# Optimization experiments

Hardware: AMD Instinct MI355X
Metric: run time of the kernel (lower is better)

The kernel has to match this reference:

```python
import jax, jax.numpy as jnp
import numpy as np

B, T, D = 2, 2048, 512
H, W = 8, 32
d = D // H


def setup_inputs() -> dict:
    key = jax.random.key(0)
    ks = jax.random.split(key, 9)
    s = 1.0 / np.sqrt(D)
    return {
        "x": jax.random.normal(ks[0], (B, T, D), dtype=jnp.float32),
        "wq": jax.random.normal(ks[1], (D, D), dtype=jnp.float32) * s,
        "bq": jnp.zeros((D,), dtype=jnp.float32),
        "wk": jax.random.normal(ks[2], (D, D), dtype=jnp.float32) * s,
        "bk": jnp.zeros((D,), dtype=jnp.float32),
        "wv": jax.random.normal(ks[3], (D, D), dtype=jnp.float32) * s,
        "bv": jnp.zeros((D,), dtype=jnp.float32),
        "wo": jax.random.normal(ks[4], (D, D), dtype=jnp.float32) * s,
        "bo": jnp.zeros((D,), dtype=jnp.float32),
    }


def _local_attn(x, wq, bq, wk, bk, wv, bv, wo, bo):
    Bx, Tx, Dx = x.shape
    # projections (weights stored as [D_in, D_out])
    Q = (x @ wq + bq).reshape(Bx, Tx, H, d).transpose(0, 2, 1, 3)  # [B,H,T,d]
    K = (x @ wk + bk).reshape(Bx, Tx, H, d).transpose(0, 2, 1, 3)
    V = (x @ wv + bv).reshape(Bx, Tx, H, d).transpose(0, 2, 1, 3)
    # zero-pad time axis by W on both sides (matches F.pad value=0; NO masking,
    # padded zero keys get score 0 and participate in softmax like the original)
    Kp = jnp.pad(K, ((0, 0), (0, 0), (W, W), (0, 0)))  # [B,H,T+2W,d]
    Vp = jnp.pad(V, ((0, 0), (0, 0), (W, W), (0, 0)))
    idx = jnp.arange(Tx)[:, None] + jnp.arange(2 * W + 1)[None, :]  # [T, 2W+1]
    K_loc = Kp[:, :, idx, :]  # [B,H,T,2W+1,d]
    V_loc = Vp[:, :, idx, :]
    scores = jnp.einsum("bhtd,bhtwd->bhtw", Q, K_loc) / jnp.sqrt(jnp.asarray(d, x.dtype))
    attn = jax.nn.softmax(scores, axis=-1)
    out = jnp.einsum("bhtw,bhtwd->bhtd", attn, V_loc)  # [B,H,T,d]
    out = out.transpose(0, 2, 1, 3).reshape(Bx, Tx, Dx)
    return out @ wo + bo


def reference(x, wq, bq, wk, bk, wv, bv, wo, bo):
    return _local_attn(x, wq, bq, wk, bk, wv, bv, wo, bo)
```

## Files before the change

### kernel.cpp

```cpp
#include <hip/hip_runtime.h>

using f16x8 = __attribute__((ext_vector_type(8))) _Float16;
using f16x4 = __attribute__((ext_vector_type(4))) _Float16;
using f32x4 = __attribute__((ext_vector_type(4))) float;

#define T_SEQ 2048
#define D_MODEL 512
#define NH 8
#define HD 64
#define NB 2
#define M_ROWS (NB * T_SEQ)

#define GLOAD_LDS16(g, l)                                              \
  __builtin_amdgcn_global_load_lds(                                    \
      (const __attribute__((address_space(1))) void*)(g),              \
      (__attribute__((address_space(3))) void*)(l), 16, 0, 0)

__global__ __launch_bounds__(256) void cvt_all(
    const float* __restrict__ x, const float* __restrict__ wq,
    const float* __restrict__ wk, const float* __restrict__ wv,
    const float* __restrict__ wo, const float* __restrict__ bq,
    const float* __restrict__ bk, const float* __restrict__ bv,
    _Float16* __restrict__ xh, _Float16* __restrict__ wT,
    float* __restrict__ bias3) {
  int bid = blockIdx.x;
  int i = threadIdx.x;
  if (bid < 2048) {
    int idx = (bid * 256 + i) * 4;
    float4 v = *(const float4*)(x + idx);
    f16x4 h;
    h[0] = (_Float16)v.x; h[1] = (_Float16)v.y;
    h[2] = (_Float16)v.z; h[3] = (_Float16)v.w;
    *(f16x4*)(xh + idx) = h;
    return;
  }
  bid -= 2048;
  const int z = bid >> 8;
  const int by = (bid >> 4) & 15;
  const int bx = bid & 15;
  const float* w = z == 0 ? wq : z == 1 ? wk : z == 2 ? wv : wo;
  __shared__ float t[32][33];
  int r0 = by * 32, c0 = bx * 32;
#pragma unroll
  for (int p = 0; p < 4; ++p) {
    int e = p * 256 + i;
    int row = e >> 5, col = e & 31;
    t[row][col] = w[(size_t)(r0 + row) * D_MODEL + c0 + col];
  }
  __syncthreads();
  _Float16* o = wT + (size_t)z * D_MODEL * D_MODEL;
#pragma unroll
  for (int p = 0; p < 4; ++p) {
    int e = p * 256 + i;
    int orow = e >> 5, ocol = e & 31;
    o[(size_t)(c0 + orow) * D_MODEL + r0 + ocol] = (_Float16)t[ocol][orow];
  }
  if (bx == 0 && by == 0 && z < 3) {
    const float* bb = z == 0 ? bq : z == 1 ? bk : bv;
#pragma unroll
    for (int p = 0; p < 2; ++p)
      bias3[z * D_MODEL + p * 256 + i] = bb[p * 256 + i];
  }
}

template <int OUT_F32>
__global__ __launch_bounds__(256) void gemm_bt(
    const _Float16* __restrict__ A, const _Float16* __restrict__ BtBase,
    const float* __restrict__ biasBase, void* outBase) {
  const int z = blockIdx.z;
  const _Float16* Bt = BtBase + (size_t)z * D_MODEL * D_MODEL;
  const float* bias = biasBase + z * D_MODEL;
  const int m0 = blockIdx.y * 128;
  const int n0 = blockIdx.x * 128;
  __shared__ _Float16 At[128 * 32];
  __shared__ _Float16 Bts[128 * 32];
  const int tid = threadIdx.x;
  const int l = tid & 63;
  const int wv = tid >> 6;
  const int wm = wv >> 1, wn = wv & 1;
  const int r16 = l & 15, g4 = l >> 4;
  f32x4 acc[4][4] = {};
  for (int k0 = 0; k0 < D_MODEL; k0 += 32) {
#pragma unroll
    for (int cc = 0; cc < 2; ++cc) {
      int c = tid + cc * 256;
      int row = c >> 2, part = c & 3;
      int wbase = (wv * 64 + cc * 256) * 8;
      GLOAD_LDS16(&A[(size_t)(m0 + row) * D_MODEL + k0 + part * 8],
                  &At[wbase]);
      GLOAD_LDS16(&Bt[(size_t)(n0 + row) * D_MODEL + k0 + part * 8],
                  &Bts[wbase]);
    }
    __syncthreads();
    f16x8 a[4], b[4];
#pragma unroll
    for (int mf = 0; mf < 4; ++mf)
      a[mf] = *(const f16x8*)&At[(wm * 64 + mf * 16 + r16) * 32 + g4 * 8];
#pragma unroll
    for (int nf = 0; nf < 4; ++nf)
      b[nf] = *(const f16x8*)&Bts[(wn * 64 + nf * 16 + r16) * 32 + g4 * 8];
#pragma unroll
    for (int mf = 0; mf < 4; ++mf)
#pragma unroll
      for (int nf = 0; nf < 4; ++nf)
        acc[mf][nf] = __builtin_amdgcn_mfma_f32_16x16x32_f16(
            a[mf], b[nf], acc[mf][nf], 0, 0, 0);
    __syncthreads();
  }
#pragma unroll
  for (int mf = 0; mf < 4; ++mf) {
#pragma unroll
    for (int nf = 0; nf < 4; ++nf) {
      int col = n0 + wn * 64 + nf * 16 + r16;
      float bs = bias[col];
#pragma unroll
      for (int r = 0; r < 4; ++r) {
        int rowi = m0 + wm * 64 + mf * 16 + g4 * 4 + r;
        float v = acc[mf][nf][r] + bs;
        if (OUT_F32)
          ((float*)outBase)[(size_t)rowi * D_MODEL + col] = v;
        else
          ((_Float16*)outBase)[(size_t)z * M_ROWS * D_MODEL +
                               (size_t)rowi * D_MODEL + col] = (_Float16)v;
      }
    }
  }
}

__global__ __launch_bounds__(256) void local_attn(
    const _Float16* __restrict__ Q, const _Float16* __restrict__ K,
    const _Float16* __restrict__ V, _Float16* __restrict__ att) {
  const int t0 = blockIdx.x * 64;
  const int h = blockIdx.y;
  const int b = blockIdx.z;
  const int k0 = t0 - 32;
  __shared__ _Float16 Qs[64 * 64];
  __shared__ _Float16 Ks[128 * 64];
  __shared__ _Float16 Vt[64 * 128];
  __shared__ _Float16 Ps[64 * 128];
  const int tid = threadIdx.x;
  const int l = tid & 63;
  const int wv = tid >> 6;
  const size_t colbase = (size_t)h * HD;
#pragma unroll
  for (int cc = 0; cc < 2; ++cc) {
    int c = tid + cc * 256;
    int row = c >> 3, part = c & 7;
    GLOAD_LDS16(&Q[(size_t)(b * T_SEQ + t0 + row) * D_MODEL + colbase + part * 8],
                &Qs[(wv * 64 + cc * 256) * 8]);
  }
  const bool interior = (k0 >= 0) && (k0 + 128 <= T_SEQ);
  if (interior) {
#pragma unroll
    for (int cc = 0; cc < 4; ++cc) {
      int c = tid + cc * 256;
      int row = c >> 3, part = c & 7;
      GLOAD_LDS16(&K[(size_t)(b * T_SEQ + k0 + row) * D_MODEL + colbase + part * 8],
                  &Ks[(wv * 64 + cc * 256) * 8]);
    }
  } else {
#pragma unroll
    for (int cc = 0; cc < 4; ++cc) {
      int c = tid + cc * 256;
      int row = c >> 3, part = c & 7;
      int t = k0 + row;
      f16x8 v = {};
      if (t >= 0 && t < T_SEQ)
        v = *(const f16x8*)&K[(size_t)(b * T_SEQ + t) * D_MODEL + colbase + part * 8];
      *(f16x8*)&Ks[row * 64 + part * 8] = v;
    }
  }
#pragma unroll
  for (int cc = 0; cc < 4; ++cc) {
    int c = tid + cc * 256;
    int row = c >> 3, part = c & 7;
    int t = k0 + row;
    f16x8 v = {};
    if (t >= 0 && t < T_SEQ)
      v = *(const f16x8*)&V[(size_t)(b * T_SEQ + t) * D_MODEL + colbase + part * 8];
#pragma unroll
    for (int j = 0; j < 8; ++j) Vt[(part * 8 + j) * 128 + row] = v[j];
  }
  __syncthreads();
  const int r16 = l & 15, g4 = l >> 4;
  f32x4 s[8] = {};
#pragma unroll
  for (int kk = 0; kk < 2; ++kk) {
    f16x8 a = *(const f16x8*)&Qs[(wv * 16 + r16) * 64 + kk * 32 + g4 * 8];
#pragma unroll
    for (int nf = 0; nf < 8; ++nf) {
      f16x8 bb = *(const f16x8*)&Ks[(nf * 16 + r16) * 64 + kk * 32 + g4 * 8];
      s[nf] = __builtin_amdgcn_mfma_f32_16x16x32_f16(a, bb, s[nf], 0, 0, 0);
    }
  }
#pragma unroll
  for (int r = 0; r < 4; ++r) {
    int ql = wv * 16 + g4 * 4 + r;
    float vals[8];
    float m = -1e30f;
#pragma unroll
    for (int nf = 0; nf < 8; ++nf) {
      int j = nf * 16 + r16;
      bool in = (j >= ql) && (j <= ql + 64);
      float sv = in ? s[nf][r] * 0.125f : -1e30f;
      vals[nf] = sv;
      m = fmaxf(m, sv);
    }
#pragma unroll
    for (int off = 1; off < 16; off <<= 1) m = fmaxf(m, __shfl_xor(m, off, 64));
    float e[8];
    float sum = 0.f;
#pragma unroll
    for (int nf = 0; nf < 8; ++nf) {
      float ev = (vals[nf] > -1e29f) ? __expf(vals[nf] - m) : 0.f;
      e[nf] = ev;
      sum += ev;
    }
#pragma unroll
    for (int off = 1; off < 16; off <<= 1) sum += __shfl_xor(sum, off, 64);
    float inv = 1.f / sum;
#pragma unroll
    for (int nf = 0; nf < 8; ++nf)
      Ps[ql * 128 + nf * 16 + r16] = (_Float16)(e[nf] * inv);
  }
  __syncthreads();
  f32x4 o[4] = {};
#pragma unroll
  for (int kk = 0; kk < 4; ++kk) {
    f16x8 a = *(const f16x8*)&Ps[(wv * 16 + r16) * 128 + kk * 32 + g4 * 8];
#pragma unroll
    for (int nf = 0; nf < 4; ++nf) {
      f16x8 bb = *(const f16x8*)&Vt[(nf * 16 + r16) * 128 + kk * 32 + g4 * 8];
      o[nf] = __builtin_amdgcn_mfma_f32_16x16x32_f16(a, bb, o[nf], 0, 0, 0);
    }
  }
#pragma unroll
  for (int nf = 0; nf < 4; ++nf)
#pragma unroll
    for (int r = 0; r < 4; ++r) {
      int row = t0 + wv * 16 + g4 * 4 + r;
      int col = nf * 16 + r16;
      att[(size_t)(b * T_SEQ + row) * D_MODEL + colbase + col] =
          (_Float16)o[nf][r];
    }
}

extern "C" void kernel_launch(void* const* d_in, const int* in_sizes, int n_in,
                              void* d_out, int out_size, void* d_ws,
                              size_t ws_size, hipStream_t stream) {
  const float* x = (const float*)d_in[0];
  const float* wq = (const float*)d_in[1];
  const float* bq = (const float*)d_in[2];
  const float* wk = (const float*)d_in[3];
  const float* bk = (const float*)d_in[4];
  const float* wv = (const float*)d_in[5];
  const float* bv = (const float*)d_in[6];
  const float* wo = (const float*)d_in[7];
  const float* bo = (const float*)d_in[8];

  char* ws = (char*)d_ws;
  _Float16* xh = (_Float16*)(ws);
  _Float16* wT = (_Float16*)(ws + (4 << 20));
  float* bias3 = (float*)(ws + (6 << 20));
  _Float16* QKV = (_Float16*)(ws + (6 << 20) + (64 << 10));
  _Float16* att = xh;

  cvt_all<<<3072, 256, 0, stream>>>(x, wq, wk, wv, wo, bq, bk, bv, xh, wT,
                                    bias3);
  gemm_bt<0><<<dim3(4, 32, 3), 256, 0, stream>>>(xh, wT, bias3, QKV);
  const _Float16* Qm = QKV;
  const _Float16* Km = QKV + (size_t)M_ROWS * D_MODEL;
  const _Float16* Vm = Km + (size_t)M_ROWS * D_MODEL;
  local_attn<<<dim3(32, 8, 2), 256, 0, stream>>>(Qm, Km, Vm, att);
  gemm_bt<1><<<dim3(4, 32, 1), 256, 0, stream>>>(
      att, wT + (size_t)3 * D_MODEL * D_MODEL, bo, d_out);
}
```

Measured before the change: 51.01 us.

## Double-buffer GEMM tiles, swizzle/pad attention LDS, shrink output GEMM tiles

The GEMM now double-buffers its LDS tiles, so the next K-slice load is issued before computing on the current one, and there is one barrier per iteration instead of two. The GEMM is templated on BM so the output projection can use 64-row tiles, launching twice as many blocks for better CU coverage. In the attention kernel, Q and K shared-memory tiles use an XOR swizzle and the Vt and Ps rows are padded to 136 elements, aiming to cut LDS bank conflicts. The cost is doubled GEMM LDS use, which may reduce occupancy, plus more complex indexing.

```diff
diff --git a/kernel.cpp b/kernel.cpp
--- a/kernel.cpp
+++ b/kernel.cpp
@@ -63,59 +63,82 @@
   }
 }
 
-template <int OUT_F32>
+template <int OUT_F32, int BM>
 __global__ __launch_bounds__(256) void gemm_bt(
     const _Float16* __restrict__ A, const _Float16* __restrict__ BtBase,
     const float* __restrict__ biasBase, void* outBase) {
+  constexpr int BN = 128;
+  constexpr int WROWS = (BM >= 128) ? 2 : 1;
+  constexpr int WCOLS = 4 / WROWS;
+  constexpr int MF = BM / WROWS / 16;
+  constexpr int NF = BN / WCOLS / 16;
+  constexpr int NT = D_MODEL / 32;
   const int z = blockIdx.z;
   const _Float16* Bt = BtBase + (size_t)z * D_MODEL * D_MODEL;
   const float* bias = biasBase + z * D_MODEL;
-  const int m0 = blockIdx.y * 128;
-  const int n0 = blockIdx.x * 128;
-  __shared__ _Float16 At[128 * 32];
-  __shared__ _Float16 Bts[128 * 32];
+  const int m0 = blockIdx.y * BM;
+  const int n0 = blockIdx.x * BN;
+  __shared__ _Float16 At[2][BM * 32];
+  __shared__ _Float16 Bts[2][BN * 32];
   const int tid = threadIdx.x;
   const int l = tid & 63;
   const int wv = tid >> 6;
-  const int wm = wv >> 1, wn = wv & 1;
+  const int wm = wv / WCOLS, wn = wv % WCOLS;
   const int r16 = l & 15, g4 = l >> 4;
-  f32x4 acc[4][4] = {};
-  for (int k0 = 0; k0 < D_MODEL; k0 += 32) {
-#pragma unroll
-    for (int cc = 0; cc < 2; ++cc) {
+  f32x4 acc[MF][NF] = {};
+
+  auto stage = [&](int bb, int k0) {
+#pragma unroll
+    for (int cc = 0; cc < BM / 64; ++cc) {
       int c = tid + cc * 256;
       int row = c >> 2, part = c & 3;
-      int wbase = (wv * 64 + cc * 256) * 8;
       GLOAD_LDS16(&A[(size_t)(m0 + row) * D_MODEL + k0 + part * 8],
-                  &At[wbase]);
+                  &At[bb][(c - l) * 8]);
+    }
+#pragma unroll
+    for (int cc = 0; cc < BN / 64; ++cc) {
+      int c = tid + cc * 256;
+      int row = c >> 2, part = c & 3;
       GLOAD_LDS16(&Bt[(size_t)(n0 + row) * D_MODEL + k0 + part * 8],
-                  &Bts[wbase]);
-    }
-    __syncthreads();
-    f16x8 a[4], b[4];
-#pragma unroll
-    for (int mf = 0; mf < 4; ++mf)
-      a[mf] = *(const f16x8*)&At[(wm * 64 + mf * 16 + r16) * 32 + g4 * 8];
-#pragma unroll
-    for (int nf = 0; nf < 4; ++nf)
-      b[nf] = *(const f16x8*)&Bts[(wn * 64 + nf * 16 + r16) * 32 + g4 * 8];
-#pragma unroll
-    for (int mf = 0; mf < 4; ++mf)
-#pragma unroll
-      for (int nf = 0; nf < 4; ++nf)
+                  &Bts[bb][(c - l) * 8]);
+    }
+  };
+  auto compute = [&](int bb) {
+    f16x8 a[MF], b[NF];
+#pragma unroll
+    for (int mf = 0; mf < MF; ++mf)
+      a[mf] = *(const f16x8*)&At[bb][(wm * (BM / WROWS) + mf * 16 + r16) * 32 +
+                                     g4 * 8];
+#pragma unroll
+    for (int nf = 0; nf < NF; ++nf)
+      b[nf] = *(const f16x8*)&Bts[bb][(wn * (BN / WCOLS) + nf * 16 + r16) * 32 +
+                                      g4 * 8];
+#pragma unroll
+    for (int mf = 0; mf < MF; ++mf)
+#pragma unroll
+      for (int nf = 0; nf < NF; ++nf)
         acc[mf][nf] = __builtin_amdgcn_mfma_f32_16x16x32_f16(
             a[mf], b[nf], acc[mf][nf], 0, 0, 0);
+  };
+
+  stage(0, 0);
+  __syncthreads();
+#pragma unroll
+  for (int t = 0; t < NT; ++t) {
+    if (t + 1 < NT) stage((t + 1) & 1, (t + 1) * 32);
+    compute(t & 1);
     __syncthreads();
   }
-#pragma unroll
-  for (int mf = 0; mf < 4; ++mf) {
-#pragma unroll
-    for (int nf = 0; nf < 4; ++nf) {
-      int col = n0 + wn * 64 + nf * 16 + r16;
+
+#pragma unroll
+  for (int mf = 0; mf < MF; ++mf) {
+#pragma unroll
+    for (int nf = 0; nf < NF; ++nf) {
+      int col = n0 + wn * (BN / WCOLS) + nf * 16 + r16;
       float bs = bias[col];
 #pragma unroll
       for (int r = 0; r < 4; ++r) {
-        int rowi = m0 + wm * 64 + mf * 16 + g4 * 4 + r;
+        int rowi = m0 + wm * (BM / WROWS) + mf * 16 + g4 * 4 + r;
         float v = acc[mf][nf][r] + bs;
         if (OUT_F32)
           ((float*)outBase)[(size_t)rowi * D_MODEL + col] = v;
@@ -136,8 +159,8 @@
   const int k0 = t0 - 32;
   __shared__ _Float16 Qs[64 * 64];
   __shared__ _Float16 Ks[128 * 64];
-  __shared__ _Float16 Vt[64 * 128];
-  __shared__ _Float16 Ps[64 * 128];
+  __shared__ _Float16 Vt[64 * 136];
+  __shared__ _Float16 Ps[64 * 136];
   const int tid = threadIdx.x;
   const int l = tid & 63;
   const int wv = tid >> 6;
@@ -146,8 +169,9 @@
   for (int cc = 0; cc < 2; ++cc) {
     int c = tid + cc * 256;
     int row = c >> 3, part = c & 7;
-    GLOAD_LDS16(&Q[(size_t)(b * T_SEQ + t0 + row) * D_MODEL + colbase + part * 8],
-                &Qs[(wv * 64 + cc * 256) * 8]);
+    int sp = part ^ (row & 7);
+    GLOAD_LDS16(&Q[(size_t)(b * T_SEQ + t0 + row) * D_MODEL + colbase + sp * 8],
+                &Qs[(c - l) * 8]);
   }
   const bool interior = (k0 >= 0) && (k0 + 128 <= T_SEQ);
   if (interior) {
@@ -155,8 +179,10 @@
     for (int cc = 0; cc < 4; ++cc) {
       int c = tid + cc * 256;
       int row = c >> 3, part = c & 7;
-      GLOAD_LDS16(&K[(size_t)(b * T_SEQ + k0 + row) * D_MODEL + colbase + part * 8],
-                  &Ks[(wv * 64 + cc * 256) * 8]);
+      int sp = part ^ (row & 7);
+      GLOAD_LDS16(
+          &K[(size_t)(b * T_SEQ + k0 + row) * D_MODEL + colbase + sp * 8],
+          &Ks[(c - l) * 8]);
     }
   } else {
 #pragma unroll
@@ -166,8 +192,9 @@
       int t = k0 + row;
       f16x8 v = {};
       if (t >= 0 && t < T_SEQ)
-        v = *(const f16x8*)&K[(size_t)(b * T_SEQ + t) * D_MODEL + colbase + part * 8];
-      *(f16x8*)&Ks[row * 64 + part * 8] = v;
+        v = *(const f16x8*)&K[(size_t)(b * T_SEQ + t) * D_MODEL + colbase +
+                              part * 8];
+      *(f16x8*)&Ks[row * 64 + (part ^ (row & 7)) * 8] = v;
     }
   }
 #pragma unroll
@@ -177,19 +204,22 @@
     int t = k0 + row;
     f16x8 v = {};
     if (t >= 0 && t < T_SEQ)
-      v = *(const f16x8*)&V[(size_t)(b * T_SEQ + t) * D_MODEL + colbase + part * 8];
-#pragma unroll
-    for (int j = 0; j < 8; ++j) Vt[(part * 8 + j) * 128 + row] = v[j];
+      v = *(const f16x8*)&V[(size_t)(b * T_SEQ + t) * D_MODEL + colbase +
+                            part * 8];
+#pragma unroll
+    for (int j = 0; j < 8; ++j) Vt[(part * 8 + j) * 136 + row] = v[j];
   }
   __syncthreads();
   const int r16 = l & 15, g4 = l >> 4;
   f32x4 s[8] = {};
 #pragma unroll
   for (int kk = 0; kk < 2; ++kk) {
-    f16x8 a = *(const f16x8*)&Qs[(wv * 16 + r16) * 64 + kk * 32 + g4 * 8];
+    int p = kk * 4 + g4;
+    f16x8 a = *(const f16x8*)&Qs[(wv * 16 + r16) * 64 + (p ^ (r16 & 7)) * 8];
 #pragma unroll
     for (int nf = 0; nf < 8; ++nf) {
-      f16x8 bb = *(const f16x8*)&Ks[(nf * 16 + r16) * 64 + kk * 32 + g4 * 8];
+      f16x8 bb =
+          *(const f16x8*)&Ks[(nf * 16 + r16) * 64 + (p ^ (r16 & 7)) * 8];
       s[nf] = __builtin_amdgcn_mfma_f32_16x16x32_f16(a, bb, s[nf], 0, 0, 0);
     }
   }
@@ -221,16 +251,16 @@
     float inv = 1.f / sum;
 #pragma unroll
     for (int nf = 0; nf < 8; ++nf)
-      Ps[ql * 128 + nf * 16 + r16] = (_Float16)(e[nf] * inv);
+      Ps[ql * 136 + nf * 16 + r16] = (_Float16)(e[nf] * inv);
   }
   __syncthreads();
   f32x4 o[4] = {};
 #pragma unroll
   for (int kk = 0; kk < 4; ++kk) {
-    f16x8 a = *(const f16x8*)&Ps[(wv * 16 + r16) * 128 + kk * 32 + g4 * 8];
+    f16x8 a = *(const f16x8*)&Ps[(wv * 16 + r16) * 136 + kk * 32 + g4 * 8];
 #pragma unroll
     for (int nf = 0; nf < 4; ++nf) {
-      f16x8 bb = *(const f16x8*)&Vt[(nf * 16 + r16) * 128 + kk * 32 + g4 * 8];
+      f16x8 bb = *(const f16x8*)&Vt[(nf * 16 + r16) * 136 + kk * 32 + g4 * 8];
       o[nf] = __builtin_amdgcn_mfma_f32_16x16x32_f16(a, bb, o[nf], 0, 0, 0);
     }
   }
@@ -267,11 +297,11 @@
 
   cvt_all<<<3072, 256, 0, stream>>>(x, wq, wk, wv, wo, bq, bk, bv, xh, wT,
                                     bias3);
-  gemm_bt<0><<<dim3(4, 32, 3), 256, 0, stream>>>(xh, wT, bias3, QKV);
+  gemm_bt<0, 128><<<dim3(4, 32, 3), 256, 0, stream>>>(xh, wT, bias3, QKV);
   const _Float16* Qm = QKV;
   const _Float16* Km = QKV + (size_t)M_ROWS * D_MODEL;
   const _Float16* Vm = Km + (size_t)M_ROWS * D_MODEL;
   local_attn<<<dim3(32, 8, 2), 256, 0, stream>>>(Qm, Km, Vm, att);
-  gemm_bt<1><<<dim3(4, 32, 1), 256, 0, stream>>>(
+  gemm_bt<1, 64><<<dim3(4, 64, 1), 256, 0, stream>>>(
       att, wT + (size_t)3 * D_MODEL * D_MODEL, bo, d_out);
 }
```

Result: faster. 47.43 us (-7.0%).
